# Optimization experiments

Hardware: AMD Instinct MI355X
Metric: run time of the kernel (lower is better)

The kernel has to match this reference:

```python
import jax, jax.numpy as jnp
import numpy as np

FILTER_SIZE = 15
BLUR_SIGMA_INIT = 5.0
DIFF_SIGMA_INIT = 1.0


def setup_inputs() -> dict:
    key = jax.random.key(0)
    x = jax.random.normal(key, (2, 3, 224, 224), dtype=jnp.float32)
    blur_sigma = jnp.float32(BLUR_SIGMA_INIT)
    diff_sigma = jnp.float32(DIFF_SIGMA_INIT)
    return {"x": x, "blur_sigma": blur_sigma, "diff_sigma": diff_sigma,
            "filter_size": FILTER_SIZE}


def _squared_distances(k, dtype):
    # distances[i, j] = (i - mid)^2 + (j - mid)^2, flattened row-major (matches unfold)
    mid = k // 2
    r = np.arange(k) - mid
    d = (r[:, None] ** 2 + r[None, :] ** 2).reshape(-1)
    return jnp.asarray(d, dtype=dtype)


def reference(x, blur_sigma, diff_sigma, filter_size):
    k = filter_size
    pad = k // 2
    B, C, H, W = x.shape
    # F.pad(x + 100, ...) - 100 == constant pad with -100
    padded = jnp.pad(x, ((0, 0), (0, 0), (pad, pad), (pad, pad)),
                     constant_values=-100.0)
    # [B, C*k*k, H, W], channel-major ordering (C, then kernel row, then kernel col)
    patches = jax.lax.conv_general_dilated_patches(
        padded, (k, k), (1, 1), 'VALID')
    patches = patches.reshape(B, C, k * k, H, W)
    dist = _squared_distances(k, x.dtype)  # [k*k]
    diffs = (patches - x[:, :, None]) ** 2 / (diff_sigma ** 2)
    blurs = dist[None, None, :, None, None] / (blur_sigma ** 2)
    # exp(-(diffs+blurs)) normalized over window axis == softmax of the negated logits
    probs = jax.nn.softmax(-(diffs + blurs), axis=2)
    return jnp.sum(patches * probs, axis=2)
```

## Files before the change

### kernel.cpp

```cpp
#include <hip/hip_runtime.h>

#define HH 224
#define WW 224
#define K 15
#define PAD 7
#define BX 32
#define BY 8
#define TW (BX + K - 1)
#define TH (BY + K - 1)
#define TSTRIDE 48

__global__ __launch_bounds__(BX * BY)
void bilateral_denoise_kernel(const float* __restrict__ x,
                              const float* __restrict__ blur_sigma_p,
                              const float* __restrict__ diff_sigma_p,
                              float* __restrict__ out)
{
    __shared__ float tile[TH * TSTRIDE];

    const int tx = threadIdx.x;
    const int ty = threadIdx.y;
    const int tid = ty * BX + tx;
    const int w0 = blockIdx.x * BX;
    const int h0 = blockIdx.y * BY;
    const int plane = blockIdx.z;

    const float* __restrict__ xp = x + (size_t)plane * HH * WW;

    for (int idx = tid; idx < TH * TW; idx += BX * BY) {
        const int r = idx / TW;
        const int c = idx - r * TW;
        const int gh = h0 - PAD + r;
        const int gw = w0 - PAD + c;
        float v = -100.0f;
        if (gh >= 0 && gh < HH && gw >= 0 && gw < WW) v = xp[gh * WW + gw];
        tile[r * TSTRIDE + c] = v;
    }
    __syncthreads();

    const float bs = blur_sigma_p[0];
    const float ds = diff_sigma_p[0];
    const float LOG2E = 1.44269504088896340736f;
    const float na  = -LOG2E / (ds * ds);
    const float nk2 = -LOG2E / (bs * bs);

    float nbj[K];
#pragma unroll
    for (int j = 0; j < K; ++j) {
        nbj[j] = (float)((j - PAD) * (j - PAD)) * nk2;
    }

    const float cv = tile[(ty + PAD) * TSTRIDE + tx + PAD];

    float wsum = 0.0f;
    float vsum = 0.0f;

#pragma unroll
    for (int i = 0; i < K; ++i) {
        const float nbi = (float)((i - PAD) * (i - PAD)) * nk2;
        const float* __restrict__ row = &tile[(ty + i) * TSTRIDE + tx];
#pragma unroll
        for (int j = 0; j < K; ++j) {
            const float v = row[j];
            const float d = v - cv;
            const float m = d * na;
            const float t = __builtin_fmaf(m, d, nbi + nbj[j]);
            const float e = __builtin_amdgcn_exp2f(t);
            wsum += e;
            vsum = __builtin_fmaf(e, v, vsum);
        }
    }

    out[(size_t)plane * HH * WW + (size_t)(h0 + ty) * WW + (w0 + tx)] = vsum / wsum;
}

extern "C" void kernel_launch(void* const* d_in, const int* in_sizes, int n_in,
                              void* d_out, int out_size, void* d_ws, size_t ws_size,
                              hipStream_t stream) {
    const float* x  = (const float*)d_in[0];
    const float* bs = (const float*)d_in[1];
    const float* ds = (const float*)d_in[2];
    float* out = (float*)d_out;

    const int planes = in_sizes[0] / (HH * WW);
    dim3 grid(WW / BX, HH / BY, planes);
    dim3 block(BX, BY, 1);
    hipLaunchKernelGGL(bilateral_denoise_kernel, grid, block, 0, stream,
                       x, bs, ds, out);
}
```

Before: 20.38 us.

## Vectorize LDS row reads with float4 and factor out the column spatial weights

Each thread now reads its row window from shared memory as five aligned float4 loads starting at a 4-aligned column. It processes 18 slots, and a per-thread table of precomputed column Gaussian weights masks the three slots that fall outside its own 15-wide window to zero. The range term is expanded algebraically into two FMAs around the center value, and the column spatial factor becomes a multiply instead of being added inside the exponent. The tile load loop is also restructured to use row/column strides. This cuts the number of LDS instructions, but it adds a fifth more exp2 evaluations plus an extra multiply per slot.

Measured after the change: 23.95 us. 1.18x slower.

```diff
diff --git a/kernel.cpp b/kernel.cpp
--- a/kernel.cpp
+++ b/kernel.cpp
@@ -9,6 +9,7 @@
 #define TW (BX + K - 1)
 #define TH (BY + K - 1)
 #define TSTRIDE 48
+#define NSLOT 18
 
 __global__ __launch_bounds__(BX * BY)
 void bilateral_denoise_kernel(const float* __restrict__ x,
@@ -16,25 +17,25 @@
                               const float* __restrict__ diff_sigma_p,
                               float* __restrict__ out)
 {
-    __shared__ float tile[TH * TSTRIDE];
+    __shared__ __align__(16) float tile[TH * TSTRIDE];
 
     const int tx = threadIdx.x;
     const int ty = threadIdx.y;
-    const int tid = ty * BX + tx;
     const int w0 = blockIdx.x * BX;
     const int h0 = blockIdx.y * BY;
     const int plane = blockIdx.z;
 
     const float* __restrict__ xp = x + (size_t)plane * HH * WW;
 
-    for (int idx = tid; idx < TH * TW; idx += BX * BY) {
-        const int r = idx / TW;
-        const int c = idx - r * TW;
-        const int gh = h0 - PAD + r;
-        const int gw = w0 - PAD + c;
-        float v = -100.0f;
-        if (gh >= 0 && gh < HH && gw >= 0 && gw < WW) v = xp[gh * WW + gw];
-        tile[r * TSTRIDE + c] = v;
+    for (int rr = ty; rr < TH; rr += BY) {
+        const int gh = h0 - PAD + rr;
+        for (int cc = tx; cc < TSTRIDE; cc += BX) {
+            const int gw = w0 - PAD + cc;
+            float v = -100.0f;
+            if (gh >= 0 && gh < HH && gw >= 0 && gw < WW && cc < TW)
+                v = xp[gh * WW + gw];
+            tile[rr * TSTRIDE + cc] = v;
+        }
     }
     __syncthreads();
 
@@ -44,30 +45,46 @@
     const float na  = -LOG2E / (ds * ds);
     const float nk2 = -LOG2E / (bs * bs);
 
-    float nbj[K];
-#pragma unroll
-    for (int j = 0; j < K; ++j) {
-        nbj[j] = (float)((j - PAD) * (j - PAD)) * nk2;
-    }
+    const int ab = tx & ~3;
+    const int p  = tx & 3;
 
     const float cv = tile[(ty + PAD) * TSTRIDE + tx + PAD];
+    const float bb  = -2.0f * na * cv;
+    const float cc2 = na * cv * cv;
+
+    const float fp = (float)p;
+    float wcol[NSLOT];
+#pragma unroll
+    for (int s = 0; s < NSLOT; ++s) {
+        const float jj = (float)(s - PAD) - fp;
+        const float wjs = __builtin_amdgcn_exp2f(jj * jj * nk2);
+        const int j = s - p;
+        wcol[s] = (j >= 0 && j < K) ? wjs : 0.0f;
+    }
 
     float wsum = 0.0f;
     float vsum = 0.0f;
 
 #pragma unroll
     for (int i = 0; i < K; ++i) {
-        const float nbi = (float)((i - PAD) * (i - PAD)) * nk2;
-        const float* __restrict__ row = &tile[(ty + i) * TSTRIDE + tx];
+        const float ci = __builtin_fmaf((float)((i - PAD) * (i - PAD)), nk2, cc2);
+        const float4* __restrict__ rp =
+            (const float4*)&tile[(ty + i) * TSTRIDE + ab];
+        float r[20];
+        *(float4*)&r[0]  = rp[0];
+        *(float4*)&r[4]  = rp[1];
+        *(float4*)&r[8]  = rp[2];
+        *(float4*)&r[12] = rp[3];
+        *(float4*)&r[16] = rp[4];
 #pragma unroll
-        for (int j = 0; j < K; ++j) {
-            const float v = row[j];
-            const float d = v - cv;
-            const float m = d * na;
-            const float t = __builtin_fmaf(m, d, nbi + nbj[j]);
+        for (int s = 0; s < NSLOT; ++s) {
+            const float v = r[s];
+            const float inner = __builtin_fmaf(v, na, bb);
+            const float t = __builtin_fmaf(v, inner, ci);
             const float e = __builtin_amdgcn_exp2f(t);
-            wsum += e;
-            vsum = __builtin_fmaf(e, v, vsum);
+            const float we = wcol[s] * e;
+            wsum += we;
+            vsum = __builtin_fmaf(we, v, vsum);
         }
     }
 
```

## Compute two vertically adjacent outputs per thread sharing row loads, factor column weights

Applied to the files above, without the earlier changes.

Each thread now produces two outputs stacked vertically, so each shared-memory row it loads feeds both accumulations, cutting LDS reads roughly in half. The exponent is rewritten as a quadratic in v with precomputed per-pixel coefficients, and the separable column blur factor is pulled out of the inner loop: per-column accumulators are scaled by exp2 of the column weight at the end. The tile load loop is restructured into row and column loops, and the grid is halved in the vertical direction. The cost is many more live registers (60 accumulators plus 15 row values), which could lower occupancy, and half as many blocks.

Result: slower. 31.76 us (+55.9%).

```diff
diff --git a/kernel.cpp b/kernel.cpp
--- a/kernel.cpp
+++ b/kernel.cpp
@@ -6,8 +6,10 @@
 #define PAD 7
 #define BX 32
 #define BY 8
+#define VO 2
+#define OROWS (BY * VO)
+#define TROWS (OROWS + K - 1)
 #define TW (BX + K - 1)
-#define TH (BY + K - 1)
 #define TSTRIDE 48
 
 __global__ __launch_bounds__(BX * BY)
@@ -16,25 +18,24 @@
                               const float* __restrict__ diff_sigma_p,
                               float* __restrict__ out)
 {
-    __shared__ float tile[TH * TSTRIDE];
+    __shared__ float tile[TROWS * TSTRIDE];
 
     const int tx = threadIdx.x;
     const int ty = threadIdx.y;
-    const int tid = ty * BX + tx;
     const int w0 = blockIdx.x * BX;
-    const int h0 = blockIdx.y * BY;
+    const int h0 = blockIdx.y * OROWS;
     const int plane = blockIdx.z;
 
     const float* __restrict__ xp = x + (size_t)plane * HH * WW;
 
-    for (int idx = tid; idx < TH * TW; idx += BX * BY) {
-        const int r = idx / TW;
-        const int c = idx - r * TW;
-        const int gh = h0 - PAD + r;
-        const int gw = w0 - PAD + c;
-        float v = -100.0f;
-        if (gh >= 0 && gh < HH && gw >= 0 && gw < WW) v = xp[gh * WW + gw];
-        tile[r * TSTRIDE + c] = v;
+    for (int rr = ty; rr < TROWS; rr += BY) {
+        const int gh = h0 - PAD + rr;
+        for (int cc = tx; cc < TW; cc += BX) {
+            const int gw = w0 - PAD + cc;
+            float v = -100.0f;
+            if (gh >= 0 && gh < HH && gw >= 0 && gw < WW) v = xp[gh * WW + gw];
+            tile[rr * TSTRIDE + cc] = v;
+        }
     }
     __syncthreads();
 
@@ -44,34 +45,66 @@
     const float na  = -LOG2E / (ds * ds);
     const float nk2 = -LOG2E / (bs * bs);
 
-    float nbj[K];
+    const int r0 = 2 * ty;
+    const float cvA = tile[(r0 + PAD)     * TSTRIDE + tx + PAD];
+    const float cvB = tile[(r0 + PAD + 1) * TSTRIDE + tx + PAD];
+    const float bbA = -2.0f * na * cvA;
+    const float ccA = na * cvA * cvA;
+    const float bbB = -2.0f * na * cvB;
+    const float ccB = na * cvB * cvB;
+
+    float awA[K], avA[K], awB[K], avB[K];
 #pragma unroll
-    for (int j = 0; j < K; ++j) {
-        nbj[j] = (float)((j - PAD) * (j - PAD)) * nk2;
-    }
-
-    const float cv = tile[(ty + PAD) * TSTRIDE + tx + PAD];
-
-    float wsum = 0.0f;
-    float vsum = 0.0f;
+    for (int j = 0; j < K; ++j) { awA[j] = 0.0f; avA[j] = 0.0f; awB[j] = 0.0f; avB[j] = 0.0f; }
 
 #pragma unroll
-    for (int i = 0; i < K; ++i) {
-        const float nbi = (float)((i - PAD) * (i - PAD)) * nk2;
-        const float* __restrict__ row = &tile[(ty + i) * TSTRIDE + tx];
+    for (int r = 0; r < 16; ++r) {
+        const float* __restrict__ row = &tile[(r0 + r) * TSTRIDE + tx];
+        float rv[K];
 #pragma unroll
-        for (int j = 0; j < K; ++j) {
-            const float v = row[j];
-            const float d = v - cv;
-            const float m = d * na;
-            const float t = __builtin_fmaf(m, d, nbi + nbj[j]);
-            const float e = __builtin_amdgcn_exp2f(t);
-            wsum += e;
-            vsum = __builtin_fmaf(e, v, vsum);
+        for (int j = 0; j < K; ++j) rv[j] = row[j];
+
+        if (r < 15) {
+            const int iA = r;
+            const float ciA = __builtin_fmaf((float)((iA - PAD) * (iA - PAD)), nk2, ccA);
+#pragma unroll
+            for (int j = 0; j < K; ++j) {
+                const float v = rv[j];
+                const float inner = __builtin_fmaf(v, na, bbA);
+                const float t = __builtin_fmaf(v, inner, ciA);
+                const float e = __builtin_amdgcn_exp2f(t);
+                awA[j] += e;
+                avA[j] = __builtin_fmaf(e, v, avA[j]);
+            }
+        }
+        if (r >= 1) {
+            const int iB = r - 1;
+            const float ciB = __builtin_fmaf((float)((iB - PAD) * (iB - PAD)), nk2, ccB);
+#pragma unroll
+            for (int j = 0; j < K; ++j) {
+                const float v = rv[j];
+                const float inner = __builtin_fmaf(v, na, bbB);
+                const float t = __builtin_fmaf(v, inner, ciB);
+                const float e = __builtin_amdgcn_exp2f(t);
+                awB[j] += e;
+                avB[j] = __builtin_fmaf(e, v, avB[j]);
+            }
         }
     }
 
-    out[(size_t)plane * HH * WW + (size_t)(h0 + ty) * WW + (w0 + tx)] = vsum / wsum;
+    float wA = 0.0f, vA = 0.0f, wB = 0.0f, vB = 0.0f;
+#pragma unroll
+    for (int j = 0; j < K; ++j) {
+        const float wj = __builtin_amdgcn_exp2f((float)((j - PAD) * (j - PAD)) * nk2);
+        wA = __builtin_fmaf(wj, awA[j], wA);
+        vA = __builtin_fmaf(wj, avA[j], vA);
+        wB = __builtin_fmaf(wj, awB[j], wB);
+        vB = __builtin_fmaf(wj, avB[j], vB);
+    }
+
+    const size_t base = (size_t)plane * HH * WW + (size_t)(h0 + 2 * ty) * WW + (w0 + tx);
+    out[base]      = vA / wA;
+    out[base + WW] = vB / wB;
 }
 
 extern "C" void kernel_launch(void* const* d_in, const int* in_sizes, int n_in,
@@ -83,7 +116,7 @@
     float* out = (float*)d_out;
 
     const int planes = in_sizes[0] / (HH * WW);
-    dim3 grid(WW / BX, HH / BY, planes);
+    dim3 grid(WW / BX, HH / OROWS, planes);
     dim3 block(BX, BY, 1);
     hipLaunchKernelGGL(bilateral_denoise_kernel, grid, block, 0, stream,
                        x, bs, ds, out);
```
